# Optimization experiments

Measured on AMD Instinct MI355X. Metric: run time of the kernel, lower is better.

The kernel has to match this reference:

```python
import jax, jax.numpy as jnp
import numpy as np

N, C, K, P, Q, PS = 32, 128, 128, 64, 64, 3

def setup_inputs() -> dict:
    key = jax.random.key(0)
    k1, k2, k3 = jax.random.split(key, 3)
    x = jax.random.normal(k1, (N, C, P, Q), dtype=jnp.float32)
    W = jax.random.normal(k2, (K, C * PS * PS), dtype=jnp.float32) * (1.0 / np.sqrt(C * PS * PS))
    perturbs = jax.random.normal(k3, (N, K, P, Q), dtype=jnp.float32)
    return {"x": x, "W": W, "perturbs": perturbs}

def reference(x, W, perturbs):
    # patchify (pad=1, unfold 3x3, stride 1) + matmul with W^T is exactly a
    # 3x3 SAME convolution: flatten order of patchify is (C, kh, kw), matching
    # conv.weight.reshape(k, -1). Express it as a direct conv (no im2col blowup).
    k = W.shape[0]
    c = x.shape[1]
    w = W.reshape(k, c, PS, PS)  # OIHW
    out = jax.lax.conv_general_dilated(
        x, w,
        window_strides=(1, 1),
        padding=((1, 1), (1, 1)),
        dimension_numbers=("NCHW", "OIHW", "NCHW"),
    )
    return out + perturbs
```

## Files before the change

kernel.cpp:

```cpp
#include <hip/hip_runtime.h>
#include <hip/hip_bf16.h>

#define NN 32
#define CCH 128
#define KK 128
#define PP 64
#define QQ 64

typedef __bf16 bf16x8 __attribute__((ext_vector_type(8)));
typedef float f32x16 __attribute__((ext_vector_type(16)));
typedef float f32x4 __attribute__((ext_vector_type(4)));

#define XT_ELEMS (32ull * 64 * 64 * 128)

__global__ __launch_bounds__(256) void prep_x(const float* __restrict__ x,
                                              __bf16* __restrict__ xT) {
    __shared__ float tile[128 * 64];
    const int t = threadIdx.x;
    const int p = blockIdx.x;
    const int n = blockIdx.y;

#pragma unroll
    for (int pass = 0; pass < 8; ++pass) {
        int idx = pass * 256 + t;
        int qf = idx & 15;
        int c  = idx >> 4;
        f32x4 v = *(const f32x4*)(x + (((size_t)n * CCH + c) * PP + p) * QQ + qf * 4);
        int key = ((c >> 3) & 15) * 4;
        *(f32x4*)(tile + c * 64 + ((qf * 4) ^ key)) = v;
    }
    __syncthreads();

#pragma unroll
    for (int pass = 0; pass < 4; ++pass) {
        int cc   = pass * 2 + (t >> 7);
        int rem  = t & 127;
        int q    = rem >> 1;
        int half = rem & 1;
        int c0   = cc * 16 + half * 8;
        int key  = ((c0 >> 3) & 15) * 4;
        bf16x8 o;
#pragma unroll
        for (int j = 0; j < 8; ++j) o[j] = (__bf16)tile[(c0 + j) * 64 + (q ^ key)];
        *(bf16x8*)(xT + ((((size_t)n * 8 + cc) * PP + p) * QQ + q) * 16 + half * 8) = o;
    }
}

__global__ __launch_bounds__(256) void prep_w(const float* __restrict__ W,
                                              __bf16* __restrict__ Wf) {
    const int id = blockIdx.x * 256 + threadIdx.x;
    const int lane = id & 63;
    const int r1   = id >> 6;
    const int kb   = r1 & 3;
    const int r2   = r1 >> 2;
    const int t    = r2 % 9;
    const int cc   = r2 / 9;

    const int k  = kb * 32 + (lane & 31);
    const int c0 = cc * 16 + (lane >> 5) * 8;

    bf16x8 o;
#pragma unroll
    for (int j = 0; j < 8; ++j)
        o[j] = (__bf16)W[(size_t)k * (CCH * 9) + (size_t)(c0 + j) * 9 + t];
    ((bf16x8*)Wf)[id] = o;
}

#define XPITCH 2112
#define XROWS  6
#define XBYTES (XROWS * XPITCH)

__global__ __launch_bounds__(256, 2) void conv_main(const __bf16* __restrict__ xT,
                                                    const __bf16* __restrict__ Wf,
                                                    const float* __restrict__ per,
                                                    float* __restrict__ out) {
    __shared__ __align__(16) char xlds[2][XBYTES];
    __shared__ __align__(16) char scr_lds[4][4096];

    const int tid  = threadIdx.x;
    const int lane = tid & 63;
    const int w    = tid >> 6;
    const int kbs  = w & 1;
    const int pb   = w >> 1;
    const int n    = blockIdx.y;
    const int p0   = blockIdx.x * 4;
    const int m    = lane & 31;
    const int half = lane >> 5;

    if (tid < 24) {
        int row = tid >> 2, part = tid & 3;
        int off = row * XPITCH + (part >> 1) * 2080 + (part & 1) * 16;
        *(f32x4*)(xlds[0] + off) = f32x4{0.f, 0.f, 0.f, 0.f};
        *(f32x4*)(xlds[1] + off) = f32x4{0.f, 0.f, 0.f, 0.f};
    }

    f32x16 acc[2][2][2];
#pragma unroll
    for (int a = 0; a < 2; ++a)
#pragma unroll
        for (int b = 0; b < 2; ++b)
#pragma unroll
            for (int c = 0; c < 2; ++c)
#pragma unroll
                for (int e = 0; e < 16; ++e) acc[a][b][c][e] = 0.f;

    const char* xb = (const char*)xT + ((size_t)n * 8) * PP * QQ * 32;

    const bf16x8* wg = (const bf16x8*)Wf + kbs * 128 + lane;

    auto stage_x = [&](int ccn, int buf) {
        const char* gx = xb + (size_t)ccn * (PP * QQ * 32);
#pragma unroll
        for (int it = 0; it < 3; ++it) {
            int gi  = it * 256 + tid;
            int row = gi >> 7;
            int wi  = (gi & 127) * 16;
            int r   = p0 - 1 + row;
            int rc  = r < 0 ? 0 : (r > 63 ? 63 : r);
            __builtin_amdgcn_global_load_lds(
                (const __attribute__((address_space(1))) unsigned int*)(gx + (size_t)rc * 2048 + wi),
                (__attribute__((address_space(3))) unsigned int*)(xlds[buf] + row * XPITCH + 32 + wi),
                16, 0, 0);
        }
    };

    auto compute = [&](int buf, int cc) {
        const char* xbase = xlds[buf];
        const bf16x8* wc = wg + (size_t)cc * 2304;

        bf16x8 a_cur[3][2], a_prev[3][2];
#pragma unroll
        for (int ri = 0; ri < 4; ++ri) {
            const int rr = pb * 2 + ri;
            const int r  = p0 + pb * 2 + ri - 1;
            const bool rok = ((unsigned)r < (unsigned)PP);

            bf16x8 b[3][2];
            if (rok) {
                const char* rbase = xbase + rr * XPITCH + half * 16;
#pragma unroll
                for (int dq = 0; dq < 3; ++dq)
#pragma unroll
                    for (int qb = 0; qb < 2; ++qb)
                        b[dq][qb] = *(const bf16x8*)(rbase + (qb * 32 + m + dq) * 32);
            }

            if (ri < 3) {
#pragma unroll
                for (int dq = 0; dq < 3; ++dq)
#pragma unroll
                    for (int kb = 0; kb < 2; ++kb)
                        a_cur[dq][kb] = wc[((ri * 3 + dq) * 4 + kb) * 64];
            }

            if (rok) {
                if (ri >= 1) {
#pragma unroll
                    for (int dq = 0; dq < 3; ++dq)
#pragma unroll
                        for (int kb = 0; kb < 2; ++kb)
#pragma unroll
                            for (int qb = 0; qb < 2; ++qb)
                                acc[1][kb][qb] = __builtin_amdgcn_mfma_f32_32x32x16_bf16(
                                    a_prev[dq][kb], b[dq][qb], acc[1][kb][qb], 0, 0, 0);
                }
                if (ri < 3) {
#pragma unroll
                    for (int dq = 0; dq < 3; ++dq)
#pragma unroll
                        for (int kb = 0; kb < 2; ++kb)
#pragma unroll
                            for (int qb = 0; qb < 2; ++qb)
                                acc[0][kb][qb] = __builtin_amdgcn_mfma_f32_32x32x16_bf16(
                                    a_cur[dq][kb], b[dq][qb], acc[0][kb][qb], 0, 0, 0);
                }
            }

            if (ri < 3) {
#pragma unroll
                for (int dq = 0; dq < 3; ++dq)
#pragma unroll
                    for (int kb = 0; kb < 2; ++kb) a_prev[dq][kb] = a_cur[dq][kb];
            }
        }
    };

    stage_x(0, 0);
    __syncthreads();

    for (int cc = 0; cc < 7; ++cc) {
        stage_x(cc + 1, (cc + 1) & 1);
        compute(cc & 1, cc);
        __syncthreads();
    }

    auto tile_addr = [&](int it, int j) -> size_t {
        int oi = it >> 2, kbi = (it >> 1) & 1, qb = it & 1;
        int prow = p0 + pb * 2 + oi;
        int k = (kbs * 2 + kbi) * 32 + (lane >> 3) + j * 8;
        int q = qb * 32 + (lane & 7) * 4;
        return (((size_t)n * KK + k) * PP + prow) * QQ + q;
    };

    float* scr = (float*)scr_lds[w];

    auto process = [&](int it, f32x4 (&pv)[4]) {
        int oi = it >> 2, kbi = (it >> 1) & 1, qb = it & 1;
        f32x16 v = acc[oi][kbi][qb];
#pragma unroll
        for (int r = 0; r < 16; ++r) {
            int kl = (r & 3) + 8 * (r >> 2) + 4 * half;
            scr[kl * 32 + ((((m >> 2) ^ (kl & 7)) << 2) | (m & 3))] = v[r];
        }
#pragma unroll
        for (int j = 0; j < 4; ++j) {
            int kl = (lane >> 3) + j * 8;
            f32x4 d = *(const f32x4*)(scr + kl * 32 + (((lane & 7) ^ (kl & 7)) << 2));
            f32x4 s = d + pv[j];
            __builtin_nontemporal_store(s, (f32x4*)(out + tile_addr(it, j)));
        }
    };

    f32x4 pv0[4], pv1[4];
#pragma unroll
    for (int j = 0; j < 4; ++j) pv0[j] = *(const f32x4*)(per + tile_addr(0, j));

    compute(1, 7);

#pragma unroll
    for (int itp = 0; itp < 4; ++itp) {
        const int itA = itp * 2, itB = itp * 2 + 1;
#pragma unroll
        for (int j = 0; j < 4; ++j) pv1[j] = *(const f32x4*)(per + tile_addr(itB, j));
        process(itA, pv0);
        if (itp < 3) {
#pragma unroll
            for (int j = 0; j < 4; ++j)
                pv0[j] = *(const f32x4*)(per + tile_addr(itA + 2, j));
        }
        process(itB, pv1);
    }
}

extern "C" void kernel_launch(void* const* d_in, const int* in_sizes, int n_in,
                              void* d_out, int out_size, void* d_ws, size_t ws_size,
                              hipStream_t stream) {
    const float* x   = (const float*)d_in[0];
    const float* W   = (const float*)d_in[1];
    const float* per = (const float*)d_in[2];
    float* out = (float*)d_out;

    __bf16* xT = (__bf16*)d_ws;
    __bf16* Wf = (__bf16*)((char*)d_ws + XT_ELEMS * 2);

    prep_x<<<dim3(PP, NN), 256, 0, stream>>>(x, xT);
    prep_w<<<dim3(72), 256, 0, stream>>>(W, Wf);
    conv_main<<<dim3(PP / 4, NN), 256, 0, stream>>>(xT, Wf, per, out);
}
```

Measured before the change: 209.6 us.

## Read input activations directly from global memory instead of LDS double buffering

Removes the LDS staging of x tiles via global_load_lds and its double-buffered pipeline with per-chunk barriers. Each wave now loads its B fragments straight from global memory (relying on L1/L2 caching), with explicit boundary masking for the padded columns. This cuts LDS usage and the barriers, but adds redundant global loads across waves and exposes load latency directly to the MFMA loop without prefetching.

```diff
diff --git a/kernel.cpp b/kernel.cpp
--- a/kernel.cpp
+++ b/kernel.cpp
@@ -66,15 +66,10 @@
     ((bf16x8*)Wf)[id] = o;
 }
 
-#define XPITCH 2112
-#define XROWS  6
-#define XBYTES (XROWS * XPITCH)
-
 __global__ __launch_bounds__(256, 2) void conv_main(const __bf16* __restrict__ xT,
                                                     const __bf16* __restrict__ Wf,
                                                     const float* __restrict__ per,
                                                     float* __restrict__ out) {
-    __shared__ __align__(16) char xlds[2][XBYTES];
     __shared__ __align__(16) char scr_lds[4][4096];
 
     const int tid  = threadIdx.x;
@@ -87,12 +82,9 @@
     const int m    = lane & 31;
     const int half = lane >> 5;
 
-    if (tid < 24) {
-        int row = tid >> 2, part = tid & 3;
-        int off = row * XPITCH + (part >> 1) * 2080 + (part & 1) * 16;
-        *(f32x4*)(xlds[0] + off) = f32x4{0.f, 0.f, 0.f, 0.f};
-        *(f32x4*)(xlds[1] + off) = f32x4{0.f, 0.f, 0.f, 0.f};
-    }
+    bf16x8 bz;
+#pragma unroll
+    for (int j = 0; j < 8; ++j) bz[j] = (__bf16)0.f;
 
     f32x16 acc[2][2][2];
 #pragma unroll
@@ -108,41 +100,29 @@
 
     const bf16x8* wg = (const bf16x8*)Wf + kbs * 128 + lane;
 
-    auto stage_x = [&](int ccn, int buf) {
-        const char* gx = xb + (size_t)ccn * (PP * QQ * 32);
-#pragma unroll
-        for (int it = 0; it < 3; ++it) {
-            int gi  = it * 256 + tid;
-            int row = gi >> 7;
-            int wi  = (gi & 127) * 16;
-            int r   = p0 - 1 + row;
-            int rc  = r < 0 ? 0 : (r > 63 ? 63 : r);
-            __builtin_amdgcn_global_load_lds(
-                (const __attribute__((address_space(1))) unsigned int*)(gx + (size_t)rc * 2048 + wi),
-                (__attribute__((address_space(3))) unsigned int*)(xlds[buf] + row * XPITCH + 32 + wi),
-                16, 0, 0);
-        }
-    };
-
-    auto compute = [&](int buf, int cc) {
-        const char* xbase = xlds[buf];
+    auto compute = [&](int cc) {
+        const char* xcc = xb + (size_t)cc * (PP * QQ * 32);
         const bf16x8* wc = wg + (size_t)cc * 2304;
 
         bf16x8 a_cur[3][2], a_prev[3][2];
 #pragma unroll
         for (int ri = 0; ri < 4; ++ri) {
-            const int rr = pb * 2 + ri;
             const int r  = p0 + pb * 2 + ri - 1;
             const bool rok = ((unsigned)r < (unsigned)PP);
 
             bf16x8 b[3][2];
             if (rok) {
-                const char* rbase = xbase + rr * XPITCH + half * 16;
+                const char* xrow = xcc + (size_t)r * 2048 + half * 16;
 #pragma unroll
                 for (int dq = 0; dq < 3; ++dq)
 #pragma unroll
-                    for (int qb = 0; qb < 2; ++qb)
-                        b[dq][qb] = *(const bf16x8*)(rbase + (qb * 32 + m + dq) * 32);
+                    for (int qb = 0; qb < 2; ++qb) {
+                        int q_in = qb * 32 + m + dq - 1;
+                        bool ok  = ((unsigned)q_in < (unsigned)QQ);
+                        int qc   = ok ? q_in : 0;
+                        bf16x8 v = *(const bf16x8*)(xrow + qc * 32);
+                        b[dq][qb] = ok ? v : bz;
+                    }
             }
 
             if (ri < 3) {
@@ -185,14 +165,7 @@
         }
     };
 
-    stage_x(0, 0);
-    __syncthreads();
-
-    for (int cc = 0; cc < 7; ++cc) {
-        stage_x(cc + 1, (cc + 1) & 1);
-        compute(cc & 1, cc);
-        __syncthreads();
-    }
+    for (int cc = 0; cc < 7; ++cc) compute(cc);
 
     auto tile_addr = [&](int it, int j) -> size_t {
         int oi = it >> 2, kbi = (it >> 1) & 1, qb = it & 1;
@@ -225,7 +198,7 @@
 #pragma unroll
     for (int j = 0; j < 4; ++j) pv0[j] = *(const f32x4*)(per + tile_addr(0, j));
 
-    compute(1, 7);
+    compute(7);
 
 #pragma unroll
     for (int itp = 0; itp < 4; ++itp) {
```

Result: slower. 214.6 us (+2.4%).

## Fuse fp32-to-bf16 input transpose into conv main loop staging

Applied to the files above, without the earlier changes.

Drops the separate prep_x kernel that converted x to a channel-blocked bf16 layout in workspace. The conv kernel now reads fp32 x directly, converts 8 channels per lane to bf16 and writes them into LDS, replacing the async global_load_lds copies. This removes one kernel launch and a full write plus re-read of the transposed tensor. In exchange, staging becomes synchronous register-path loads, and each block re-reads and re-converts its halo rows, which may expose more latency inside the double-buffered loop.

```diff
diff --git a/kernel.cpp b/kernel.cpp
--- a/kernel.cpp
+++ b/kernel.cpp
@@ -11,40 +11,6 @@
 typedef float f32x16 __attribute__((ext_vector_type(16)));
 typedef float f32x4 __attribute__((ext_vector_type(4)));
 
-#define XT_ELEMS (32ull * 64 * 64 * 128)
-
-__global__ __launch_bounds__(256) void prep_x(const float* __restrict__ x,
-                                              __bf16* __restrict__ xT) {
-    __shared__ float tile[128 * 64];
-    const int t = threadIdx.x;
-    const int p = blockIdx.x;
-    const int n = blockIdx.y;
-
-#pragma unroll
-    for (int pass = 0; pass < 8; ++pass) {
-        int idx = pass * 256 + t;
-        int qf = idx & 15;
-        int c  = idx >> 4;
-        f32x4 v = *(const f32x4*)(x + (((size_t)n * CCH + c) * PP + p) * QQ + qf * 4);
-        int key = ((c >> 3) & 15) * 4;
-        *(f32x4*)(tile + c * 64 + ((qf * 4) ^ key)) = v;
-    }
-    __syncthreads();
-
-#pragma unroll
-    for (int pass = 0; pass < 4; ++pass) {
-        int cc   = pass * 2 + (t >> 7);
-        int rem  = t & 127;
-        int q    = rem >> 1;
-        int half = rem & 1;
-        int c0   = cc * 16 + half * 8;
-        int key  = ((c0 >> 3) & 15) * 4;
-        bf16x8 o;
-#pragma unroll
-        for (int j = 0; j < 8; ++j) o[j] = (__bf16)tile[(c0 + j) * 64 + (q ^ key)];
-        *(bf16x8*)(xT + ((((size_t)n * 8 + cc) * PP + p) * QQ + q) * 16 + half * 8) = o;
-    }
-}
 
 __global__ __launch_bounds__(256) void prep_w(const float* __restrict__ W,
                                               __bf16* __restrict__ Wf) {
@@ -70,7 +36,7 @@
 #define XROWS  6
 #define XBYTES (XROWS * XPITCH)
 
-__global__ __launch_bounds__(256, 2) void conv_main(const __bf16* __restrict__ xT,
+__global__ __launch_bounds__(256, 2) void conv_main(const float* __restrict__ x,
                                                     const __bf16* __restrict__ Wf,
                                                     const float* __restrict__ per,
                                                     float* __restrict__ out) {
@@ -104,25 +70,27 @@
 #pragma unroll
                 for (int e = 0; e < 16; ++e) acc[a][b][c][e] = 0.f;
 
-    const char* xb = (const char*)xT + ((size_t)n * 8) * PP * QQ * 32;
-
-    const bf16x8* wg = (const bf16x8*)Wf + kbs * 128 + lane;
-
-    auto stage_x = [&](int ccn, int buf) {
-        const char* gx = xb + (size_t)ccn * (PP * QQ * 32);
+    const float* xn = x + (size_t)n * CCH * PP * QQ;
+
+    auto stage = [&](int ccn, int buf) {
+        const float* xs = xn + (size_t)ccn * 16 * PP * QQ;
 #pragma unroll
         for (int it = 0; it < 3; ++it) {
-            int gi  = it * 256 + tid;
-            int row = gi >> 7;
-            int wi  = (gi & 127) * 16;
+            int t4  = it * 4 + w;
+            int row = t4 >> 1;
+            int ch  = t4 & 1;
             int r   = p0 - 1 + row;
             int rc  = r < 0 ? 0 : (r > 63 ? 63 : r);
-            __builtin_amdgcn_global_load_lds(
-                (const __attribute__((address_space(1))) unsigned int*)(gx + (size_t)rc * 2048 + wi),
-                (__attribute__((address_space(3))) unsigned int*)(xlds[buf] + row * XPITCH + 32 + wi),
-                16, 0, 0);
-        }
-    };
+            const float* src = xs + ((size_t)(ch * 8) * PP + rc) * QQ + lane;
+            bf16x8 o;
+#pragma unroll
+            for (int j = 0; j < 8; ++j)
+                o[j] = (__bf16)src[(size_t)j * PP * QQ];
+            *(bf16x8*)(xlds[buf] + row * XPITCH + 32 + lane * 32 + ch * 16) = o;
+        }
+    };
+
+    const bf16x8* wg = (const bf16x8*)Wf + kbs * 128 + lane;
 
     auto compute = [&](int buf, int cc) {
         const char* xbase = xlds[buf];
@@ -185,11 +153,11 @@
         }
     };
 
-    stage_x(0, 0);
+    stage(0, 0);
     __syncthreads();
 
     for (int cc = 0; cc < 7; ++cc) {
-        stage_x(cc + 1, (cc + 1) & 1);
+        stage(cc + 1, (cc + 1) & 1);
         compute(cc & 1, cc);
         __syncthreads();
     }
@@ -250,10 +218,8 @@
     const float* per = (const float*)d_in[2];
     float* out = (float*)d_out;
 
-    __bf16* xT = (__bf16*)d_ws;
-    __bf16* Wf = (__bf16*)((char*)d_ws + XT_ELEMS * 2);
-
-    prep_x<<<dim3(PP, NN), 256, 0, stream>>>(x, xT);
+    __bf16* Wf = (__bf16*)d_ws;
+
     prep_w<<<dim3(72), 256, 0, stream>>>(W, Wf);
-    conv_main<<<dim3(PP / 4, NN), 256, 0, stream>>>(xT, Wf, per, out);
+    conv_main<<<dim3(PP / 4, NN), 256, 0, stream>>>(x, Wf, per, out);
 }
```

New measurement: 193.1 us. -7.8%, faster.
